# Performance work log

Hardware: AMD Instinct MI355X
Metric: run time of the kernel (lower is better)

Reference implementation:

```python
import jax, jax.numpy as jnp
import numpy as np

B, C_IN, N, T = 16, 2, 207, 12
E = 1863
EMB = 64
HEADS = 8
F_DIM = EMB * T  # 768


def setup_inputs() -> dict:
    key = jax.random.key(0)
    ks = jax.random.split(key, 12)
    s = 0.05
    x = jax.random.normal(ks[0], (B, C_IN, N, T), jnp.float32)
    src = jax.random.randint(ks[1], (E,), 0, N)
    dst = jax.random.randint(ks[2], (E,), 0, N)
    # ensure every node has an incoming edge (self loops in the tail)
    loop = jnp.arange(N)
    src = src.at[-N:].set(loop)
    dst = dst.at[-N:].set(loop)
    Ws = jax.random.normal(ks[3], (EMB, C_IN), jnp.float32) * s
    bs = jnp.zeros((EMB,), jnp.float32)
    Wc = jax.random.normal(ks[4], (EMB, C_IN), jnp.float32) * s
    bc = jnp.zeros((EMB,), jnp.float32)
    W1 = jax.random.normal(ks[5], (F_DIM, HEADS * F_DIM), jnp.float32) * s
    al1 = jax.random.normal(ks[6], (HEADS, F_DIM), jnp.float32) * s
    ar1 = jax.random.normal(ks[7], (HEADS, F_DIM), jnp.float32) * s
    b1 = jnp.zeros((HEADS, F_DIM), jnp.float32)
    W2 = jax.random.normal(ks[8], (F_DIM, HEADS * F_DIM), jnp.float32) * s
    al2 = jax.random.normal(ks[9], (HEADS, F_DIM), jnp.float32) * s
    ar2 = jax.random.normal(ks[10], (HEADS, F_DIM), jnp.float32) * s
    b2 = jnp.zeros((HEADS, F_DIM), jnp.float32)
    return dict(x=x, src=src, dst=dst, Ws=Ws, bs=bs, Wc=Wc, bc=bc,
                W1=W1, al1=al1, ar1=ar1, b1=b1, W2=W2, al2=al2, ar2=ar2, b2=b2)


def _gat_layer(h, W, al, ar, b, src, dst):
    # h: [B, N, F]  (dropout disabled: eval-mode reference)
    feat = (h @ W).reshape(B, N, HEADS, F_DIM)          # [B,N,H,F]
    el = jnp.einsum('bnhf,hf->bnh', feat, al)           # src scores
    er = jnp.einsum('bnhf,hf->bnh', feat, ar)           # dst scores
    e = jax.nn.leaky_relu(el[:, src] + er[:, dst], 0.2)  # [B,E,H]

    def edge_softmax(ev):  # ev: [E,H], softmax over edges sharing a dst node
        m = jax.ops.segment_max(ev, dst, num_segments=N)
        ex = jnp.exp(ev - m[dst])
        denom = jax.ops.segment_sum(ex, dst, num_segments=N)
        return ex / denom[dst]

    alpha = jax.vmap(edge_softmax)(e)                   # [B,E,H]
    msg = alpha[..., None] * feat[:, src]               # [B,E,H,F]
    rst = jax.vmap(lambda m_: jax.ops.segment_sum(m_, dst, num_segments=N))(msg)
    rst = jax.nn.elu(rst + b)                            # bias + F.elu activation
    return rst.mean(axis=2)                              # mean over heads -> [B,N,F]


def reference(x, src, dst, Ws, bs, Wc, bc, W1, al1, ar1, b1, W2, al2, ar2, b2):
    # 1x1 convs == channel matmuls
    x1 = jnp.einsum('bcnt,oc->bont', x, Ws) + bs[None, :, None, None]
    x2 = jax.nn.leaky_relu(jnp.einsum('bcnt,oc->bont', x, Wc) + bc[None, :, None, None], 0.01)
    xm = x1 + x2                                         # [B,EMB,N,T]
    h = xm.transpose(0, 2, 1, 3).reshape(B, N, F_DIM)    # [B,N,768]
    h = _gat_layer(h, W1, al1, ar1, b1, src, dst)
    h = _gat_layer(h, W2, al2, ar2, b2, src, dst)
    gc = h.reshape(B, N, EMB, T).transpose(0, 2, 1, 3)   # [B,EMB,N,T]
    return xm + gc
```

## Files before the change

kernel.cpp:

```cpp
#include <hip/hip_runtime.h>

#define BB 16
#define NNODE 207
#define TTS 12
#define NE 1863
#define NEP2 1920
#define NH 8
#define FD 768
#define HFD 6144
#define MM 3312
#define MP 3328

typedef short bf16x8 __attribute__((ext_vector_type(8)));
typedef float f32x4 __attribute__((ext_vector_type(4)));

typedef __attribute__((address_space(3))) unsigned int lds_u32;
typedef __attribute__((address_space(1))) const unsigned int glb_u32;

__device__ __forceinline__ unsigned short f2b(float f) {
    unsigned int u = __float_as_uint(f);
    u = (u + 0x7FFFu + ((u >> 16) & 1u)) >> 16;
    return (unsigned short)u;
}
__device__ __forceinline__ float b2f(unsigned short b) {
    return __uint_as_float(((unsigned int)b) << 16);
}

#define CSR_EBLK 468
__global__ __launch_bounds__(256) void prep_misc(const float* __restrict__ W1,
                                                 const float* __restrict__ al1, const float* __restrict__ ar1,
                                                 const float* __restrict__ W2,
                                                 const float* __restrict__ al2, const float* __restrict__ ar2,
                                                 float* __restrict__ wlr,
                                                 unsigned short* __restrict__ Wt1,
                                                 unsigned short* __restrict__ Wt2,
                                                 const int* __restrict__ dst,
                                                 int* __restrict__ ptr, int* __restrict__ cidx) {
    __shared__ __align__(16) char smem[16640];
    const int bid = blockIdx.x;
    const int t = threadIdx.x;
    const int wv = t >> 6, lane = t & 63;
    if (bid < 3072) {
        const int wid = bid * 4 + wv;
        const int which = wid / 6144;
        const int r = wid % 6144;
        const int k = r >> 3, hh = r & 7;
        const float* W = which ? W2 : W1;
        const float* al = which ? al2 : al1;
        const float* ar = which ? ar2 : ar1;
        const float4* wp = (const float4*)(W + (size_t)k * HFD + hh * FD);
        const float4* ap = (const float4*)(al + hh * FD);
        const float4* rp = (const float4*)(ar + hh * FD);
        float sl = 0.f, sr = 0.f;
#pragma unroll
        for (int jj = 0; jj < 3; jj++) {
            int j = lane + jj * 64;
            float4 w = wp[j], a = ap[j], b = rp[j];
            sl += w.x * a.x + w.y * a.y + w.z * a.z + w.w * a.w;
            sr += w.x * b.x + w.y * b.y + w.z * b.z + w.w * b.w;
        }
#pragma unroll
        for (int off = 32; off > 0; off >>= 1) {
            sl += __shfl_down(sl, off);
            sr += __shfl_down(sr, off);
        }
        if (lane == 0) {
            wlr[(size_t)which * 12288 + 0 + hh * FD + k] = sl;
            wlr[(size_t)which * 12288 + 6144 + hh * FD + k] = sr;
        }
    } else if (bid < 5376) {
        float (*tile)[65] = (float(*)[65])smem;
        const int idx = bid - 3072;
        const int which = idx / 1152;
        const int r2 = idx % 1152;
        const int k0 = (r2 % 12) * 64;
        const int n0 = (r2 / 12) * 64;
        const float* W = which ? W2 : W1;
        unsigned short* Wt = which ? Wt2 : Wt1;
        const int c = t & 63, r0 = t >> 6;
#pragma unroll
        for (int i = 0; i < 16; i++) {
            int r = r0 + i * 4;
            tile[r][c] = W[(size_t)(k0 + r) * HFD + n0 + c];
        }
        __syncthreads();
#pragma unroll
        for (int i = 0; i < 16; i++) {
            int r = r0 + i * 4;
            Wt[(size_t)(n0 + r) * FD + k0 + c] = f2b(tile[c][r]);
        }
    } else {
        int* dl = (int*)smem;
        const int b2 = bid - 5376;
        for (int i = t; i < NEP2; i += 256) dl[i] = (i < NE) ? dst[i] : 0x0FFFFFFF;
        __syncthreads();
        if (b2 < CSR_EBLK) {
            const int e = b2 * 4 + wv;
            if (e >= NE) return;
            const int d = dl[e];
            int pos = 0;
#pragma unroll
            for (int j = 0; j < 30; j++) {
                int i = lane + j * 64;
                int di = dl[i];
                pos += (int)(di < d) + (int)((i < e) & (di == d));
            }
#pragma unroll
            for (int off = 32; off > 0; off >>= 1) pos += __shfl_down(pos, off);
            if (lane == 0) cidx[pos] = e;
        } else {
            const int n = (b2 - CSR_EBLK) * 4 + wv;
            if (n > NNODE) return;
            int cnt = 0;
#pragma unroll
            for (int j = 0; j < 30; j++) cnt += (int)(dl[lane + j * 64] < n);
#pragma unroll
            for (int off = 32; off > 0; off >>= 1) cnt += __shfl_down(cnt, off);
            if (lane == 0) ptr[n] = cnt;
        }
    }
}

__global__ __launch_bounds__(256) void prep_h(const float* __restrict__ x,
                                              const float* __restrict__ Ws, const float* __restrict__ bs,
                                              const float* __restrict__ Wc, const float* __restrict__ bc,
                                              const float* __restrict__ wl, const float* __restrict__ wr,
                                              const int* __restrict__ src, const int* __restrict__ cidx,
                                              int* __restrict__ esrc,
                                              float* __restrict__ h0, unsigned short* __restrict__ hbf,
                                              float* __restrict__ el, float* __restrict__ er) {
    __shared__ float redl[4][8], redr[4][8];
    const int bn = blockIdx.x;
    const int t = threadIdx.x;
    if (bn >= MP) {
        int p = (bn - MP) * 256 + t;
        if (p < NE) esrc[p] = src[cidx[p]];
        return;
    }
    if (bn >= MM) {
#pragma unroll
        for (int c = 0; c < 3; c++) hbf[(size_t)bn * FD + c * 256 + t] = 0;
        return;
    }
    const int b = bn / NNODE, n = bn % NNODE;
    float pl[8] = {}, pr[8] = {};
#pragma unroll
    for (int c = 0; c < 3; c++) {
        int idx = c * 256 + t;
        int e = idx / TTS, tt = idx % TTS;
        float x0 = x[((size_t)(b * 2 + 0) * NNODE + n) * TTS + tt];
        float x1 = x[((size_t)(b * 2 + 1) * NNODE + n) * TTS + tt];
        float s1 = Ws[e * 2] * x0 + Ws[e * 2 + 1] * x1 + bs[e];
        float s2 = Wc[e * 2] * x0 + Wc[e * 2 + 1] * x1 + bc[e];
        s2 = s2 > 0.f ? s2 : 0.01f * s2;
        float v = s1 + s2;
        h0[(size_t)bn * FD + idx] = v;
        hbf[(size_t)bn * FD + idx] = f2b(v);
#pragma unroll
        for (int hh = 0; hh < 8; hh++) {
            pl[hh] += v * wl[hh * FD + idx];
            pr[hh] += v * wr[hh * FD + idx];
        }
    }
    const int wv = t >> 6, lane = t & 63;
#pragma unroll
    for (int hh = 0; hh < 8; hh++) {
        float a = pl[hh], c2 = pr[hh];
#pragma unroll
        for (int off = 32; off > 0; off >>= 1) {
            a += __shfl_down(a, off);
            c2 += __shfl_down(c2, off);
        }
        if (lane == 0) { redl[wv][hh] = a; redr[wv][hh] = c2; }
    }
    __syncthreads();
    if (t < 8) {
        el[bn * NH + t] = redl[0][t] + redl[1][t] + redl[2][t] + redl[3][t];
        er[bn * NH + t] = redr[0][t] + redr[1][t] + redr[2][t] + redr[3][t];
    }
}

__global__ __launch_bounds__(256) void gemm_bf16(const unsigned short* __restrict__ A,
                                                 const unsigned short* __restrict__ Bt,
                                                 unsigned short* __restrict__ C) {
    __shared__ __align__(16) unsigned short Alds[128 * 64];
    __shared__ __align__(16) unsigned short Blds[128 * 64];
    const int t = threadIdx.x;
    const int lane = t & 63;
    const int wv = t >> 6;
    const int wr = (wv >> 1) * 64, wc = (wv & 1) * 64;
    const int mt = blockIdx.y * 128, nt = blockIdx.x * 128;
    const int lm = lane & 15;
    const int s4 = lane >> 4;
    const int sl0 = ((0 + s4) ^ (lm & 7)) * 8;
    const int sl1 = ((4 + s4) ^ (lm & 7)) * 8;

    const int rr = lane >> 3;
    const int ssl = ((lane & 7) ^ rr) * 8;
    const unsigned short* ap[4];
    const unsigned short* bp[4];
#pragma unroll
    for (int q = 0; q < 4; q++) {
        int row = wv * 32 + q * 8 + rr;
        ap[q] = A + (size_t)(mt + row) * FD + ssl;
        bp[q] = Bt + (size_t)(nt + row) * FD + ssl;
    }

    f32x4 acc[4][4] = {};
    for (int ks = 0; ks < FD; ks += 64) {
#pragma unroll
        for (int q = 0; q < 4; q++) {
            __builtin_amdgcn_global_load_lds((glb_u32*)(ap[q] + ks),
                (lds_u32*)(Alds + (wv * 4 + q) * 512), 16, 0, 0);
            __builtin_amdgcn_global_load_lds((glb_u32*)(bp[q] + ks),
                (lds_u32*)(Blds + (wv * 4 + q) * 512), 16, 0, 0);
        }
        __syncthreads();
        {
            bf16x8 af[4], bfv[4];
#pragma unroll
            for (int i = 0; i < 4; i++)
                af[i] = *(const bf16x8*)(Alds + (wr + i * 16 + lm) * 64 + sl0);
#pragma unroll
            for (int j = 0; j < 4; j++)
                bfv[j] = *(const bf16x8*)(Blds + (wc + j * 16 + lm) * 64 + sl0);
#pragma unroll
            for (int i = 0; i < 4; i++)
#pragma unroll
                for (int j = 0; j < 4; j++)
                    acc[i][j] = __builtin_amdgcn_mfma_f32_16x16x32_bf16(af[i], bfv[j], acc[i][j], 0, 0, 0);
        }
        {
            bf16x8 af[4], bfv[4];
#pragma unroll
            for (int i = 0; i < 4; i++)
                af[i] = *(const bf16x8*)(Alds + (wr + i * 16 + lm) * 64 + sl1);
#pragma unroll
            for (int j = 0; j < 4; j++)
                bfv[j] = *(const bf16x8*)(Blds + (wc + j * 16 + lm) * 64 + sl1);
#pragma unroll
            for (int i = 0; i < 4; i++)
#pragma unroll
                for (int j = 0; j < 4; j++)
                    acc[i][j] = __builtin_amdgcn_mfma_f32_16x16x32_bf16(af[i], bfv[j], acc[i][j], 0, 0, 0);
        }
        __syncthreads();
    }
    const int rbase = s4 * 4;
#pragma unroll
    for (int i = 0; i < 4; i++) {
#pragma unroll
        for (int r = 0; r < 4; r++) {
            int grow = mt + wr + i * 16 + rbase + r;
            if (grow < MM) {
#pragma unroll
                for (int j = 0; j < 4; j++) {
                    int gcol = nt + wc + j * 16 + lm;
                    C[(size_t)grow * HFD + gcol] = f2b(acc[i][j][r]);
                }
            }
        }
    }
}

template <int LAST>
__global__ __launch_bounds__(256) void msg_agg(const unsigned short* __restrict__ feat,
                                               const int* __restrict__ cptr, const int* __restrict__ esrc,
                                               const float* __restrict__ bias,
                                               const float* __restrict__ el_in, const float* __restrict__ er_in,
                                               unsigned short* __restrict__ hbf_out,
                                               const float* __restrict__ wl, const float* __restrict__ wr,
                                               float* __restrict__ el_out, float* __restrict__ er_out,
                                               const float* __restrict__ h0, float* __restrict__ out) {
    __shared__ float rstl[HFD];
    __shared__ int src_l[32];
    __shared__ float alph[32][NH];
    __shared__ float redl[4][8], redr[4][8];
    __shared__ float sm_m[8], sm_i[8], sm_er[8];
    const int bn = (blockIdx.x & 7) * (MM / 8) + (blockIdx.x >> 3);
    const int b = bn / NNODE, n = bn % NNODE;
    const int t = threadIdx.x;
    const int p0 = cptr[n], p1 = cptr[n + 1];
    const int deg = p1 - p0;
    if (t < 64) {
        const int h = t & 7, js = t >> 3;
        const float erv = er_in[(b * NNODE + n) * NH + h];
        float m = -1e30f, d = 0.f;
        for (int jb = 0; jb < deg; jb += 8) {
            int j = jb + js;
            float s = -1e30f, add = 0.f;
            if (j < deg) {
                int sn = esrc[p0 + j];
                s = el_in[(b * NNODE + sn) * NH + h] + erv;
                s = s > 0.f ? s : 0.2f * s;
                add = 1.f;
            }
            float mn = fmaxf(m, s);
            d = d * __expf(m - mn) + add * __expf(s - mn);
            m = mn;
        }
#pragma unroll
        for (int o = 8; o < 64; o <<= 1) {
            float mo = __shfl_xor(m, o), dd = __shfl_xor(d, o);
            float mn = fmaxf(m, mo);
            d = d * __expf(m - mn) + dd * __expf(mo - mn);
            m = mn;
        }
        if (js == 0) { sm_m[h] = m; sm_i[h] = 1.f / d; sm_er[h] = erv; }
    }
    __syncthreads();

    const int h0i = t / 96, h1i = (256 + t) / 96, h2i = (512 + t) / 96;
    float acc[3][8] = {};
    for (int base = p0; base < p1; base += 32) {
        const int cnt = min(32, p1 - base);
        if (t < cnt) src_l[t] = esrc[base + t];
        {
            int j = t >> 3, hh = t & 7;
            if (j < cnt) {
                float s = el_in[(b * NNODE + esrc[base + j]) * NH + hh] + sm_er[hh];
                s = s > 0.f ? s : 0.2f * s;
                alph[j][hh] = __expf(s - sm_m[hh]) * sm_i[hh];
            }
        }
        __syncthreads();
        const unsigned short* fp = feat + (size_t)(b * NNODE + src_l[0]) * HFD;
        uint4 c0 = *(const uint4*)(fp + (size_t)(0 * 256 + t) * 8);
        uint4 c1 = *(const uint4*)(fp + (size_t)(1 * 256 + t) * 8);
        uint4 c2 = *(const uint4*)(fp + (size_t)(2 * 256 + t) * 8);
        for (int j2 = 0; j2 < cnt; j2++) {
            uint4 n0, n1, n2;
            if (j2 + 1 < cnt) {
                const unsigned short* np = feat + (size_t)(b * NNODE + src_l[j2 + 1]) * HFD;
                n0 = *(const uint4*)(np + (size_t)(0 * 256 + t) * 8);
                n1 = *(const uint4*)(np + (size_t)(1 * 256 + t) * 8);
                n2 = *(const uint4*)(np + (size_t)(2 * 256 + t) * 8);
            }
            const float a0 = alph[j2][h0i], a1 = alph[j2][h1i], a2 = alph[j2][h2i];
            unsigned int w;
            w = c0.x; acc[0][0] += a0 * b2f((unsigned short)w); acc[0][1] += a0 * b2f((unsigned short)(w >> 16));
            w = c0.y; acc[0][2] += a0 * b2f((unsigned short)w); acc[0][3] += a0 * b2f((unsigned short)(w >> 16));
            w = c0.z; acc[0][4] += a0 * b2f((unsigned short)w); acc[0][5] += a0 * b2f((unsigned short)(w >> 16));
            w = c0.w; acc[0][6] += a0 * b2f((unsigned short)w); acc[0][7] += a0 * b2f((unsigned short)(w >> 16));
            w = c1.x; acc[1][0] += a1 * b2f((unsigned short)w); acc[1][1] += a1 * b2f((unsigned short)(w >> 16));
            w = c1.y; acc[1][2] += a1 * b2f((unsigned short)w); acc[1][3] += a1 * b2f((unsigned short)(w >> 16));
            w = c1.z; acc[1][4] += a1 * b2f((unsigned short)w); acc[1][5] += a1 * b2f((unsigned short)(w >> 16));
            w = c1.w; acc[1][6] += a1 * b2f((unsigned short)w); acc[1][7] += a1 * b2f((unsigned short)(w >> 16));
            w = c2.x; acc[2][0] += a2 * b2f((unsigned short)w); acc[2][1] += a2 * b2f((unsigned short)(w >> 16));
            w = c2.y; acc[2][2] += a2 * b2f((unsigned short)w); acc[2][3] += a2 * b2f((unsigned short)(w >> 16));
            w = c2.z; acc[2][4] += a2 * b2f((unsigned short)w); acc[2][5] += a2 * b2f((unsigned short)(w >> 16));
            w = c2.w; acc[2][6] += a2 * b2f((unsigned short)w); acc[2][7] += a2 * b2f((unsigned short)(w >> 16));
            c0 = n0; c1 = n1; c2 = n2;
        }
        __syncthreads();
    }
#pragma unroll
    for (int c = 0; c < 3; c++) {
        int v = c * 256 + t;
#pragma unroll
        for (int u = 0; u < 8; u++) rstl[v * 8 + u] = acc[c][u];
    }
    __syncthreads();
    float pl[8] = {}, pr[8] = {};
#pragma unroll
    for (int q = 0; q < 3; q++) {
        int f = q * 256 + t;
        float val = 0.f;
#pragma unroll
        for (int hh = 0; hh < 8; hh++) {
            float r = rstl[hh * FD + f] + bias[hh * FD + f];
            val += (r > 0.f) ? r : (expf(r) - 1.f);
        }
        val *= 0.125f;
        if (LAST) {
            int e_ = f / TTS, tt_ = f % TTS;
            out[((size_t)(b * 64 + e_) * NNODE + n) * TTS + tt_] = h0[(size_t)bn * FD + f] + val;
        } else {
            hbf_out[(size_t)bn * FD + f] = f2b(val);
#pragma unroll
            for (int hh = 0; hh < 8; hh++) {
                pl[hh] += val * wl[hh * FD + f];
                pr[hh] += val * wr[hh * FD + f];
            }
        }
    }
    if (!LAST) {
        const int wv = t >> 6, lane = t & 63;
#pragma unroll
        for (int hh = 0; hh < 8; hh++) {
            float a = pl[hh], c2 = pr[hh];
#pragma unroll
            for (int off = 32; off > 0; off >>= 1) {
                a += __shfl_down(a, off);
                c2 += __shfl_down(c2, off);
            }
            if (lane == 0) { redl[wv][hh] = a; redr[wv][hh] = c2; }
        }
        __syncthreads();
        if (t < 8) {
            el_out[bn * NH + t] = redl[0][t] + redl[1][t] + redl[2][t] + redl[3][t];
            er_out[bn * NH + t] = redr[0][t] + redr[1][t] + redr[2][t] + redr[3][t];
        }
    }
}

extern "C" void kernel_launch(void* const* d_in, const int* in_sizes, int n_in,
                              void* d_out, int out_size, void* d_ws, size_t ws_size,
                              hipStream_t stream) {
    const float* x = (const float*)d_in[0];
    const int* src = (const int*)d_in[1];
    const int* dst = (const int*)d_in[2];
    const float* Ws = (const float*)d_in[3];
    const float* bs = (const float*)d_in[4];
    const float* Wc = (const float*)d_in[5];
    const float* bc = (const float*)d_in[6];
    const float* W1 = (const float*)d_in[7];
    const float* al1 = (const float*)d_in[8];
    const float* ar1 = (const float*)d_in[9];
    const float* b1 = (const float*)d_in[10];
    const float* W2 = (const float*)d_in[11];
    const float* al2 = (const float*)d_in[12];
    const float* ar2 = (const float*)d_in[13];
    const float* b2 = (const float*)d_in[14];
    float* out = (float*)d_out;

    char* w = (char*)d_ws;
    size_t off = 0;
    auto alloc = [&](size_t bytes) -> void* {
        void* p = w + off;
        off = (off + bytes + 255) & ~(size_t)255;
        return p;
    };
    float* h0 = (float*)alloc((size_t)MM * FD * 4);
    unsigned short* hbf = (unsigned short*)alloc((size_t)MP * FD * 2);
    unsigned short* Wt1 = (unsigned short*)alloc((size_t)HFD * FD * 2);
    unsigned short* Wt2 = (unsigned short*)alloc((size_t)HFD * FD * 2);
    unsigned short* feat = (unsigned short*)alloc((size_t)MM * HFD * 2);
    float* el = (float*)alloc((size_t)MM * NH * 4);
    float* er = (float*)alloc((size_t)MM * NH * 4);
    float* el2 = (float*)alloc((size_t)MM * NH * 4);
    float* er2 = (float*)alloc((size_t)MM * NH * 4);
    int* cptr = (int*)alloc((NNODE + 1) * 4);
    int* cidx = (int*)alloc(NE * 4);
    int* esrc = (int*)alloc(NE * 4);
    float* wlr = (float*)alloc((size_t)4 * 6144 * 4);
    float* wl1 = wlr, * wr1 = wlr + 6144, * wl2 = wlr + 12288, * wr2 = wlr + 18432;

    prep_misc<<<5896, 256, 0, stream>>>(W1, al1, ar1, W2, al2, ar2, wlr, Wt1, Wt2, dst, cptr, cidx);
    prep_h<<<MP + 8, 256, 0, stream>>>(x, Ws, bs, Wc, bc, wl1, wr1, src, cidx, esrc, h0, hbf, el, er);

    gemm_bf16<<<dim3(48, 26), 256, 0, stream>>>(hbf, Wt1, feat);
    msg_agg<0><<<MM, 256, 0, stream>>>(feat, cptr, esrc, b1, el, er, hbf, wl2, wr2, el2, er2, nullptr, nullptr);

    gemm_bf16<<<dim3(48, 26), 256, 0, stream>>>(hbf, Wt2, feat);
    msg_agg<1><<<MM, 256, 0, stream>>>(feat, cptr, esrc, b2, el2, er2, nullptr, nullptr, nullptr, nullptr, nullptr, h0, out);
}
```

Before: 200.7 us.

## Double-buffer GEMM LDS tiles with K=32 stages and prefetch next tile

The bf16 GEMM now uses two LDS buffers of 128x32 per operand instead of one 128x64 buffer. It prefetches the next K-slice with global_load_lds while the current slice feeds MFMA, using a partial vmcnt wait and raw barriers. The aim is to overlap global-to-LDS transfer with matrix compute, at the cost of twice as many loop iterations and barriers and a new swizzle pattern. On the last iteration it issues a redundant reload of the final slice.

```diff
diff --git a/kernel.cpp b/kernel.cpp
--- a/kernel.cpp
+++ b/kernel.cpp
@@ -183,68 +183,59 @@
 __global__ __launch_bounds__(256) void gemm_bf16(const unsigned short* __restrict__ A,
                                                  const unsigned short* __restrict__ Bt,
                                                  unsigned short* __restrict__ C) {
-    __shared__ __align__(16) unsigned short Alds[128 * 64];
-    __shared__ __align__(16) unsigned short Blds[128 * 64];
+    __shared__ __align__(16) unsigned short Alds[2][128 * 32];
+    __shared__ __align__(16) unsigned short Blds[2][128 * 32];
     const int t = threadIdx.x;
     const int lane = t & 63;
     const int wv = t >> 6;
     const int wr = (wv >> 1) * 64, wc = (wv & 1) * 64;
     const int mt = blockIdx.y * 128, nt = blockIdx.x * 128;
     const int lm = lane & 15;
+    const int rsw = (lm >> 1) & 3;
     const int s4 = lane >> 4;
-    const int sl0 = ((0 + s4) ^ (lm & 7)) * 8;
-    const int sl1 = ((4 + s4) ^ (lm & 7)) * 8;
-
-    const int rr = lane >> 3;
-    const int ssl = ((lane & 7) ^ rr) * 8;
-    const unsigned short* ap[4];
-    const unsigned short* bp[4];
-#pragma unroll
-    for (int q = 0; q < 4; q++) {
-        int row = wv * 32 + q * 8 + rr;
-        ap[q] = A + (size_t)(mt + row) * FD + ssl;
-        bp[q] = Bt + (size_t)(nt + row) * FD + ssl;
-    }
+    const int rdoff = (s4 ^ rsw) * 8;
+
+    const int r0 = (wv * 2) * 16 + (lane >> 2);
+    const int r1 = (wv * 2 + 1) * 16 + (lane >> 2);
+    const int cseg = (((lane & 3) ^ ((lane >> 3) & 3)) * 8);
+    const unsigned short* ap0 = A + (size_t)(mt + r0) * FD + cseg;
+    const unsigned short* ap1 = A + (size_t)(mt + r1) * FD + cseg;
+    const unsigned short* bp0 = Bt + (size_t)(nt + r0) * FD + cseg;
+    const unsigned short* bp1 = Bt + (size_t)(nt + r1) * FD + cseg;
+    const int ldo0 = (wv * 2) * 512;
+    const int ldo1 = (wv * 2 + 1) * 512;
 
     f32x4 acc[4][4] = {};
-    for (int ks = 0; ks < FD; ks += 64) {
-#pragma unroll
-        for (int q = 0; q < 4; q++) {
-            __builtin_amdgcn_global_load_lds((glb_u32*)(ap[q] + ks),
-                (lds_u32*)(Alds + (wv * 4 + q) * 512), 16, 0, 0);
-            __builtin_amdgcn_global_load_lds((glb_u32*)(bp[q] + ks),
-                (lds_u32*)(Blds + (wv * 4 + q) * 512), 16, 0, 0);
-        }
-        __syncthreads();
-        {
-            bf16x8 af[4], bfv[4];
-#pragma unroll
-            for (int i = 0; i < 4; i++)
-                af[i] = *(const bf16x8*)(Alds + (wr + i * 16 + lm) * 64 + sl0);
+    __builtin_amdgcn_global_load_lds((glb_u32*)(ap0), (lds_u32*)(Alds[0] + ldo0), 16, 0, 0);
+    __builtin_amdgcn_global_load_lds((glb_u32*)(ap1), (lds_u32*)(Alds[0] + ldo1), 16, 0, 0);
+    __builtin_amdgcn_global_load_lds((glb_u32*)(bp0), (lds_u32*)(Blds[0] + ldo0), 16, 0, 0);
+    __builtin_amdgcn_global_load_lds((glb_u32*)(bp1), (lds_u32*)(Blds[0] + ldo1), 16, 0, 0);
+
+    int cur = 0;
+#pragma unroll 1
+    for (int ks = 0; ks < FD; ks += 32) {
+        const int kn = (ks + 32 < FD) ? ks + 32 : ks;
+        __builtin_amdgcn_global_load_lds((glb_u32*)(ap0 + kn), (lds_u32*)(Alds[cur ^ 1] + ldo0), 16, 0, 0);
+        __builtin_amdgcn_global_load_lds((glb_u32*)(ap1 + kn), (lds_u32*)(Alds[cur ^ 1] + ldo1), 16, 0, 0);
+        __builtin_amdgcn_global_load_lds((glb_u32*)(bp0 + kn), (lds_u32*)(Blds[cur ^ 1] + ldo0), 16, 0, 0);
+        __builtin_amdgcn_global_load_lds((glb_u32*)(bp1 + kn), (lds_u32*)(Blds[cur ^ 1] + ldo1), 16, 0, 0);
+        asm volatile("s_waitcnt vmcnt(4)" ::: "memory");
+        __builtin_amdgcn_s_barrier();
+        asm volatile("" ::: "memory");
+        bf16x8 af[4], bfv[4];
+#pragma unroll
+        for (int i = 0; i < 4; i++)
+            af[i] = *(const bf16x8*)(Alds[cur] + (wr + i * 16 + lm) * 32 + rdoff);
+#pragma unroll
+        for (int j = 0; j < 4; j++)
+            bfv[j] = *(const bf16x8*)(Blds[cur] + (wc + j * 16 + lm) * 32 + rdoff);
+#pragma unroll
+        for (int i = 0; i < 4; i++)
 #pragma unroll
             for (int j = 0; j < 4; j++)
-                bfv[j] = *(const bf16x8*)(Blds + (wc + j * 16 + lm) * 64 + sl0);
-#pragma unroll
-            for (int i = 0; i < 4; i++)
-#pragma unroll
-                for (int j = 0; j < 4; j++)
-                    acc[i][j] = __builtin_amdgcn_mfma_f32_16x16x32_bf16(af[i], bfv[j], acc[i][j], 0, 0, 0);
-        }
-        {
-            bf16x8 af[4], bfv[4];
-#pragma unroll
-            for (int i = 0; i < 4; i++)
-                af[i] = *(const bf16x8*)(Alds + (wr + i * 16 + lm) * 64 + sl1);
-#pragma unroll
-            for (int j = 0; j < 4; j++)
-                bfv[j] = *(const bf16x8*)(Blds + (wc + j * 16 + lm) * 64 + sl1);
-#pragma unroll
-            for (int i = 0; i < 4; i++)
-#pragma unroll
-                for (int j = 0; j < 4; j++)
-                    acc[i][j] = __builtin_amdgcn_mfma_f32_16x16x32_bf16(af[i], bfv[j], acc[i][j], 0, 0, 0);
-        }
-        __syncthreads();
+                acc[i][j] = __builtin_amdgcn_mfma_f32_16x16x32_bf16(af[i], bfv[j], acc[i][j], 0, 0, 0);
+        __builtin_amdgcn_s_barrier();
+        cur ^= 1;
     }
     const int rbase = s4 * 4;
 #pragma unroll
```

Result: no change. 204.5 us (+1.9%).
